# Performance work log

Measured on AMD Instinct MI355X. Metric: run time of the kernel, lower is better.

## Reference

```python
import jax, jax.numpy as jnp
import numpy as np

N_NODES = 50000
N_EDGES = 800000
NODE_IN = 10
EDGE_IN = 7
H = 128
N_LAYERS = 6
OUT_DIM = 3


def setup_inputs() -> dict:
    key = jax.random.key(0)
    ks = jax.random.split(key, 32)
    s = 0.05
    inp = {
        "x": jax.random.normal(ks[0], (N_NODES, NODE_IN), jnp.float32),
        "edge_attr": jax.random.normal(ks[1], (N_EDGES, EDGE_IN), jnp.float32),
        "edge_index": jax.random.randint(ks[2], (2, N_EDGES), 0, N_NODES, jnp.int32),
        "bc_disp": jax.random.uniform(ks[3], (N_NODES, 1), jnp.float32),
        "bc_rot": jax.random.uniform(ks[4], (N_NODES, 1), jnp.float32),
        # node encoder: MLP(10, [H], H)
        "ne_w1": jax.random.normal(ks[5], (NODE_IN, H), jnp.float32) * s,
        "ne_b1": jnp.zeros((H,), jnp.float32),
        "ne_w2": jax.random.normal(ks[6], (H, H), jnp.float32) * s,
        "ne_b2": jnp.zeros((H,), jnp.float32),
        # edge encoder: MLP(7, [H], H)
        "ee_w1": jax.random.normal(ks[7], (EDGE_IN, H), jnp.float32) * s,
        "ee_b1": jnp.zeros((H,), jnp.float32),
        "ee_w2": jax.random.normal(ks[8], (H, H), jnp.float32) * s,
        "ee_b2": jnp.zeros((H,), jnp.float32),
        # 6 GraphNetworkLayers: edge model (3H -> H), node model (2H -> H)
        "mp_ew": jax.random.normal(ks[9], (N_LAYERS, 3 * H, H), jnp.float32) * s,
        "mp_eb": jnp.zeros((N_LAYERS, H), jnp.float32),
        "mp_nw": jax.random.normal(ks[10], (N_LAYERS, 2 * H, H), jnp.float32) * s,
        "mp_nb": jnp.zeros((N_LAYERS, H), jnp.float32),
        "d_w1": jax.random.normal(ks[11], (H, H), jnp.float32) * s,
        "d_b1": jnp.zeros((H,), jnp.float32),
        "d_w2": jax.random.normal(ks[12], (H, 64), jnp.float32) * s,
        "d_b2": jnp.zeros((64,), jnp.float32),
        "d_w3": jax.random.normal(ks[13], (64, OUT_DIM), jnp.float32) * (s * 5.0),
        "d_b3": jnp.full((OUT_DIM,), 0.5, jnp.float32),
    }
    return inp


def reference(x, edge_attr, edge_index, bc_disp, bc_rot,
              ne_w1, ne_b1, ne_w2, ne_b2,
              ee_w1, ee_b1, ee_w2, ee_b2,
              mp_ew, mp_eb, mp_nw, mp_nb,
              d_w1, d_b1, d_w2, d_b2, d_w3, d_b3):
    # encode nodes and edges (Linear -> ReLU -> Linear)
    h = jax.nn.relu(x @ ne_w1 + ne_b1) @ ne_w2 + ne_b2            # [N, H]
    e = jax.nn.relu(edge_attr @ ee_w1 + ee_b1) @ ee_w2 + ee_b2    # [E, H]
    src = edge_index[0]
    dst = edge_index[1]
    # 6 residual message-passing layers: gather -> edge MLP -> scatter-add -> node MLP
    for l in range(N_LAYERS):
        msg_in = jnp.concatenate([h[src], h[dst], e], axis=-1)    # [E, 3H]
        msg = jax.nn.relu(msg_in @ mp_ew[l] + mp_eb[l])           # [E, H]
        agg = jax.ops.segment_sum(msg, dst, num_segments=N_NODES)  # [N, H] (aggr='add')
        upd = jax.nn.relu(jnp.concatenate([h, agg], axis=-1) @ mp_nw[l] + mp_nb[l])
        h = h + upd                                               # residual
    # decode: Linear -> ReLU -> Linear -> ReLU -> Linear
    z = jax.nn.relu(h @ d_w1 + d_b1)
    z = jax.nn.relu(z @ d_w2 + d_b2)
    pred = z @ d_w3 + d_b3                                        # [N, 3]
    # hard boundary conditions
    pred = jnp.concatenate([pred[:, 0:2] * (1.0 - bc_disp),
                            pred[:, 2:3] * (1.0 - bc_rot)], axis=-1)
    return pred
```

## Files before the change

kernel.cpp:

```cpp
#include <hip/hip_runtime.h>
#include <hip/hip_bf16.h>

#define NN 50000
#define NE 800000
#define H 128

typedef __hip_bfloat16 bf16;
typedef __attribute__((ext_vector_type(8))) short short8v;
typedef __attribute__((ext_vector_type(4))) float f32x4;

static __device__ __forceinline__ unsigned short f2bf_bits(float x) {
  union { __hip_bfloat16 b; unsigned short u; } cv;
  cv.b = __float2bfloat16(x);
  return cv.u;
}

__global__ __launch_bounds__(256) void zero_counts_kernel(int* __restrict__ counts) {
  int i = blockIdx.x * 256 + threadIdx.x;
  if (i < NN) counts[i] = 0;
}

__global__ __launch_bounds__(256) void hist_kernel(const int* __restrict__ dstI,
                                                   int* __restrict__ counts) {
  int e = blockIdx.x * 256 + threadIdx.x;
  if (e < NE) atomicAdd(&counts[dstI[e]], 1);
}

__global__ __launch_bounds__(256) void scan_kernel(const int* __restrict__ counts,
                                                   int* __restrict__ cursor) {
  __shared__ int sdata[256];
  __shared__ int sbase;
  const int t = threadIdx.x;
  if (t == 0) sbase = 0;
  __syncthreads();
  for (int c0 = 0; c0 < NN; c0 += 256) {
    int i = c0 + t;
    int v = (i < NN) ? counts[i] : 0;
    sdata[t] = v;
    __syncthreads();
    #pragma unroll
    for (int off = 1; off < 256; off <<= 1) {
      int x = (t >= off) ? sdata[t - off] : 0;
      __syncthreads();
      sdata[t] += x;
      __syncthreads();
    }
    if (i < NN) cursor[i] = sbase + sdata[t] - v;
    __syncthreads();
    if (t == 255) sbase += sdata[255];
    __syncthreads();
  }
}

__global__ __launch_bounds__(256) void scatter_kernel(
    const float* __restrict__ ea, const int* __restrict__ srcI, const int* __restrict__ dstI,
    int* __restrict__ cursor, bf16* __restrict__ eap,
    int* __restrict__ srcp, int* __restrict__ dstp) {
  int e = blockIdx.x * 256 + threadIdx.x;
  if (e >= NE) return;
  int d = dstI[e];
  int pos = atomicAdd(&cursor[d], 1);
  srcp[pos] = srcI[e];
  dstp[pos] = d;
  #pragma unroll
  for (int k = 0; k < 7; ++k) eap[(size_t)pos * 7 + k] = __float2bfloat16(ea[(size_t)e * 7 + k]);
}

__global__ __launch_bounds__(256) void fuse_w3_kernel(
    const float* __restrict__ ee_w2, const float* __restrict__ ee_b2,
    const float* __restrict__ mp_ew, const float* __restrict__ mp_eb,
    float* __restrict__ W3p, float* __restrict__ c3)
{
  const int l = blockIdx.x >> 3;
  const int cc = (blockIdx.x & 7) * 16;
  __shared__ float sA[H * H];
  __shared__ float sB[H * 16];
  const float* W3 = mp_ew + (size_t)l * 384 * H + 256 * H;
  for (int i = threadIdx.x; i < H * H; i += 256) sA[i] = ee_w2[i];
  for (int i = threadIdx.x; i < H * 16; i += 256) {
    int k = i >> 4, j = i & 15;
    sB[i] = W3[k * H + cc + j];
  }
  __syncthreads();
  float* out = W3p + (size_t)l * H * H;
  for (int i = threadIdx.x; i < H * 16; i += 256) {
    int r = i >> 4, j = i & 15;
    float acc = 0.f;
    #pragma unroll 8
    for (int k = 0; k < H; ++k) acc += sA[r * H + k] * sB[k * 16 + j];
    out[r * H + cc + j] = acc;
  }
  if (threadIdx.x < 16) {
    int j = threadIdx.x;
    float acc = mp_eb[l * H + cc + j];
    for (int k = 0; k < H; ++k) acc += ee_b2[k] * sB[k * 16 + j];
    c3[l * H + cc + j] = acc;
  }
}

__global__ __launch_bounds__(256) void repack_w_kernel(
    const float* __restrict__ src0, size_t lstride, bf16* __restrict__ dst0, int K)
{
  const int l = blockIdx.x;
  const float* src = src0 + (size_t)l * lstride;
  bf16* dst = dst0 + (size_t)l * K * 128;
  const int nkk = K / 32;
  const int nslots = 8 * nkk * 64;
  for (int idx = threadIdx.x; idx < nslots; idx += 256) {
    int ng = idx / (nkk * 64);
    int rem = idx % (nkk * 64);
    int kk = rem / 64, ln = rem % 64;
    #pragma unroll
    for (int j = 0; j < 8; ++j) {
      int k = kk * 32 + ((ln >> 4) * 8) + j;
      int col = ng * 16 + (ln & 15);
      dst[(size_t)idx * 8 + j] = __float2bfloat16(src[(size_t)k * 128 + col]);
    }
  }
}

__global__ __launch_bounds__(256) void node_encoder_kernel(
    const float* __restrict__ in,
    const float* __restrict__ w1, const float* __restrict__ b1,
    const float* __restrict__ w2, const float* __restrict__ b2,
    float* __restrict__ out, int nrows)
{
  __shared__ float sw1[10 * H];
  __shared__ float sw2[H * H];
  __shared__ float sb1[H];
  __shared__ float sb2[H];
  __shared__ float sin_[8][10];
  __shared__ float st[8][H];

  for (int i = threadIdx.x; i < 10 * H; i += 256) sw1[i] = w1[i];
  for (int i = threadIdx.x; i < H * H; i += 256) sw2[i] = w2[i];
  if (threadIdx.x < H) { sb1[threadIdx.x] = b1[threadIdx.x]; sb2[threadIdx.x] = b2[threadIdx.x]; }
  __syncthreads();

  const int c = threadIdx.x & 127;
  const int hf = threadIdx.x >> 7;

  for (long long r0 = (long long)blockIdx.x * 8; r0 < nrows; r0 += (long long)gridDim.x * 8) {
    if (threadIdx.x < 80) {
      int j = threadIdx.x / 10, k = threadIdx.x % 10;
      long long r = r0 + j;
      sin_[j][k] = (r < nrows) ? in[r * 10 + k] : 0.f;
    }
    __syncthreads();
    #pragma unroll
    for (int t = 0; t < 4; ++t) {
      int idx = threadIdx.x + t * 256;
      int j = idx >> 7, k = idx & 127;
      float acc = sb1[k];
      #pragma unroll
      for (int i = 0; i < 10; ++i) acc += sin_[j][i] * sw1[i * H + k];
      st[j][k] = fmaxf(acc, 0.f);
    }
    __syncthreads();
    float a0 = sb2[c], a1 = a0, a2 = a0, a3 = a0;
    #pragma unroll 4
    for (int k4 = 0; k4 < H; k4 += 4) {
      float w0 = sw2[(k4 + 0) * H + c];
      float w1v = sw2[(k4 + 1) * H + c];
      float w2v = sw2[(k4 + 2) * H + c];
      float w3v = sw2[(k4 + 3) * H + c];
      float4 s0 = *(const float4*)&st[hf * 4 + 0][k4];
      float4 s1 = *(const float4*)&st[hf * 4 + 1][k4];
      float4 s2 = *(const float4*)&st[hf * 4 + 2][k4];
      float4 s3 = *(const float4*)&st[hf * 4 + 3][k4];
      a0 += s0.x * w0 + s0.y * w1v + s0.z * w2v + s0.w * w3v;
      a1 += s1.x * w0 + s1.y * w1v + s1.z * w2v + s1.w * w3v;
      a2 += s2.x * w0 + s2.y * w1v + s2.z * w2v + s2.w * w3v;
      a3 += s3.x * w0 + s3.y * w1v + s3.z * w2v + s3.w * w3v;
    }
    float accs[4] = {a0, a1, a2, a3};
    #pragma unroll
    for (int j = 0; j < 4; ++j) {
      long long r = r0 + hf * 4 + j;
      if (r < nrows) out[r * H + c] = accs[j];
    }
    __syncthreads();
  }
}

__global__ __launch_bounds__(512) void node_AB_kernel(
    const float* __restrict__ h, const float* __restrict__ W1f, const float* __restrict__ W2f,
    bf16* __restrict__ A, bf16* __restrict__ B, float* __restrict__ agg, int nrows)
{
  __shared__ float sw1[H * H];
  __shared__ float sw2[H * H];
  __shared__ float sh[16][H];
  for (int i = threadIdx.x; i < H * H; i += 512) { sw1[i] = W1f[i]; sw2[i] = W2f[i]; }
  __syncthreads();
  const int c = threadIdx.x & 127;
  const int q = threadIdx.x >> 7;
  for (long long r0 = (long long)blockIdx.x * 16; r0 < nrows; r0 += (long long)gridDim.x * 16) {
    #pragma unroll
    for (int t = 0; t < 4; ++t) {
      int idx = threadIdx.x + t * 512;
      int j = idx >> 7, k = idx & 127;
      long long r = r0 + j;
      sh[j][k] = (r < nrows) ? h[r * H + k] : 0.f;
    }
    __syncthreads();
    float aA[4] = {0, 0, 0, 0}, aB[4] = {0, 0, 0, 0};
    #pragma unroll 2
    for (int k4 = 0; k4 < H; k4 += 4) {
      float w10 = sw1[(k4 + 0) * H + c], w11 = sw1[(k4 + 1) * H + c];
      float w12 = sw1[(k4 + 2) * H + c], w13 = sw1[(k4 + 3) * H + c];
      float w20 = sw2[(k4 + 0) * H + c], w21 = sw2[(k4 + 1) * H + c];
      float w22 = sw2[(k4 + 2) * H + c], w23 = sw2[(k4 + 3) * H + c];
      #pragma unroll
      for (int j = 0; j < 4; ++j) {
        float4 s = *(const float4*)&sh[q * 4 + j][k4];
        aA[j] += s.x * w10 + s.y * w11 + s.z * w12 + s.w * w13;
        aB[j] += s.x * w20 + s.y * w21 + s.z * w22 + s.w * w23;
      }
    }
    #pragma unroll
    for (int j = 0; j < 4; ++j) {
      long long r = r0 + q * 4 + j;
      if (r < nrows) {
        A[r * H + c] = __float2bfloat16(aA[j]);
        B[r * H + c] = __float2bfloat16(aB[j]);
        agg[r * H + c] = 0.f;
      }
    }
    __syncthreads();
  }
}

__global__ __launch_bounds__(512) void edge_mfma_scatter(
    const bf16* __restrict__ eap,
    const int* __restrict__ srcp, const int* __restrict__ dstp,
    const bf16* __restrict__ A, const bf16* __restrict__ B,
    const float* __restrict__ ew1, const float* __restrict__ eb1,
    const bf16* __restrict__ W3b, const float* __restrict__ c3,
    float* __restrict__ agg, int nE)
{
  __shared__ float sew1[7 * H];
  __shared__ float seb1[H];
  __shared__ float sea[64][8];
  __shared__ int   sidx[64];
  __shared__ int   didx[64];
  __shared__ unsigned int shid[64 * 64];
  __shared__ bf16  sAld[64][136];

  for (int i = threadIdx.x; i < 7 * H; i += 512) sew1[i] = ew1[i];
  if (threadIdx.x < H) seb1[threadIdx.x] = eb1[threadIdx.x];

  const int t = threadIdx.x;
  const int lane = t & 63;
  const int wid = t >> 6;
  const int hm = wid >> 2;
  const int colbase = (wid & 3) * 32;

  short8v bfrag[2][4];
  float c3v[2];
  #pragma unroll
  for (int n = 0; n < 2; ++n) {
    c3v[n] = c3[colbase + n * 16 + (lane & 15)];
    int ng = (colbase >> 4) + n;
    #pragma unroll
    for (int kk = 0; kk < 4; ++kk) {
      const bf16* p = W3b + ((size_t)(ng * 4 + kk) * 64 + lane) * 8;
      bfrag[n][kk] = *(const short8v*)p;
    }
  }
  __syncthreads();

  for (long long e0 = (long long)blockIdx.x * 64; e0 < nE; e0 += (long long)gridDim.x * 64) {
    if (t < 448) sea[t / 7][t % 7] = __bfloat162float(eap[e0 * 7 + t]);
    else         sidx[t - 448] = srcp[e0 + (t - 448)];
    if (t < 64)  didx[t] = dstp[e0 + t];
    __syncthreads();

    #pragma unroll
    for (int i = 0; i < 2; ++i) {
      int idx = t + i * 512;
      int el = idx >> 4, seg = idx & 15;
      int s = sidx[el];
      *(short8v*)&sAld[el][seg * 8] = *(const short8v*)&A[(size_t)s * H + seg * 8];
    }

    {
      const int e = t >> 3;
      float r0 = sea[e][0], r1 = sea[e][1], r2 = sea[e][2], r3 = sea[e][3];
      float r4 = sea[e][4], r5 = sea[e][5], r6 = sea[e][6];
      #pragma unroll
      for (int p = 0; p < 8; ++p) {
        int k2 = (t & 7) + 8 * p;
        int k = k2 * 2;
        float a0 = seb1[k], a1 = seb1[k + 1];
        a0 += r0 * sew1[0 * H + k] + r1 * sew1[1 * H + k] + r2 * sew1[2 * H + k]
            + r3 * sew1[3 * H + k] + r4 * sew1[4 * H + k] + r5 * sew1[5 * H + k]
            + r6 * sew1[6 * H + k];
        a1 += r0 * sew1[0 * H + k + 1] + r1 * sew1[1 * H + k + 1] + r2 * sew1[2 * H + k + 1]
            + r3 * sew1[3 * H + k + 1] + r4 * sew1[4 * H + k + 1] + r5 * sew1[5 * H + k + 1]
            + r6 * sew1[6 * H + k + 1];
        a0 = fmaxf(a0, 0.f); a1 = fmaxf(a1, 0.f);
        unsigned int w = (unsigned int)f2bf_bits(a0) | ((unsigned int)f2bf_bits(a1) << 16);
        int off = (e * 256 + k2 * 4) ^ ((e & 7) << 4);
        shid[off >> 2] = w;
      }
    }
    __syncthreads();

    f32x4 acc[2][2];
    const f32x4 z = {0.f, 0.f, 0.f, 0.f};
    acc[0][0] = z; acc[0][1] = z; acc[1][0] = z; acc[1][1] = z;
    #pragma unroll
    for (int m = 0; m < 2; ++m) {
      #pragma unroll
      for (int kk = 0; kk < 4; ++kk) {
        int row = hm * 32 + m * 16 + (lane & 15);
        int off = (row * 256 + kk * 64 + (lane >> 4) * 16) ^ ((row & 7) << 4);
        short8v afrag = *(const short8v*)((const char*)shid + off);
        acc[m][0] = __builtin_amdgcn_mfma_f32_16x16x32_bf16(afrag, bfrag[0][kk], acc[m][0], 0, 0, 0);
        acc[m][1] = __builtin_amdgcn_mfma_f32_16x16x32_bf16(afrag, bfrag[1][kk], acc[m][1], 0, 0, 0);
      }
    }

    const int col0 = colbase + (lane & 15);
    const int col1 = col0 + 16;
    #pragma unroll
    for (int m = 0; m < 2; ++m) {
      float vs0 = 0.f, vs1 = 0.f;
      float b0 = 0.f, b1 = 0.f;
      int dprev = -1;
      #pragma unroll
      for (int r = 0; r < 4; ++r) {
        int el = hm * 32 + m * 16 + (lane >> 4) * 4 + r;
        int d = didx[el];
        if (d != dprev) {
          if (dprev >= 0) {
            atomicAdd(&agg[(size_t)dprev * H + col0], vs0);
            atomicAdd(&agg[(size_t)dprev * H + col1], vs1);
          }
          vs0 = 0.f; vs1 = 0.f;
          b0 = __bfloat162float(B[(size_t)d * H + col0]);
          b1 = __bfloat162float(B[(size_t)d * H + col1]);
          dprev = d;
        }
        float a0v = __bfloat162float(sAld[el][col0]);
        float a1v = __bfloat162float(sAld[el][col1]);
        vs0 += fmaxf(acc[m][0][r] + c3v[0] + a0v + b0, 0.f);
        vs1 += fmaxf(acc[m][1][r] + c3v[1] + a1v + b1, 0.f);
      }
      atomicAdd(&agg[(size_t)dprev * H + col0], vs0);
      atomicAdd(&agg[(size_t)dprev * H + col1], vs1);
    }
    __syncthreads();
  }
}

template<int DO_AB>
__global__ __launch_bounds__(256) void fused_update_kernel(
    float* __restrict__ h, const float* __restrict__ aggin,
    const bf16* __restrict__ Wnb, const float* __restrict__ nb,
    const bf16* __restrict__ W1b, const bf16* __restrict__ W2b,
    bf16* __restrict__ A, bf16* __restrict__ B, float* __restrict__ aggz,
    int nrows)
{
  __shared__ unsigned int sKw[32 * 128];
  unsigned short* shnew = (unsigned short*)sKw;

  const int t = threadIdx.x;
  const int lane = t & 63;
  const int wid = t >> 6;
  const int colbase = wid * 32;

  short8v bU[2][8];
  float nbv[2];
  #pragma unroll
  for (int n = 0; n < 2; ++n) {
    int ng = wid * 2 + n;
    nbv[n] = nb[colbase + n * 16 + (lane & 15)];
    #pragma unroll
    for (int kk = 0; kk < 8; ++kk)
      bU[n][kk] = *(const short8v*)(Wnb + ((size_t)(ng * 8 + kk) * 64 + lane) * 8);
  }

  const int ntiles = (nrows + 31) / 32;
  for (int tile = blockIdx.x; tile < ntiles; tile += gridDim.x) {
    const int r0 = tile * 32;
    #pragma unroll
    for (int i = 0; i < 16; ++i) {
      int w = t + i * 256;
      int row = w >> 7, k2 = w & 127;
      int r = r0 + row;
      float v0 = 0.f, v1 = 0.f;
      if (r < nrows) {
        if (k2 < 64) { float2 p = *(const float2*)&h[(size_t)r * H + 2 * k2]; v0 = p.x; v1 = p.y; }
        else         { float2 p = *(const float2*)&aggin[(size_t)r * H + 2 * k2 - 128]; v0 = p.x; v1 = p.y; }
      }
      unsigned int wrd = (unsigned int)f2bf_bits(v0) | ((unsigned int)f2bf_bits(v1) << 16);
      sKw[((w * 4) ^ ((row & 7) << 4)) >> 2] = wrd;
    }
    __syncthreads();

    f32x4 acc[2][2];
    const f32x4 z = {0.f, 0.f, 0.f, 0.f};
    acc[0][0] = z; acc[0][1] = z; acc[1][0] = z; acc[1][1] = z;
    #pragma unroll
    for (int kk = 0; kk < 8; ++kk) {
      #pragma unroll
      for (int m = 0; m < 2; ++m) {
        int row = m * 16 + (lane & 15);
        int off = (row * 512 + kk * 64 + (lane >> 4) * 16) ^ ((row & 7) << 4);
        short8v afrag = *(const short8v*)((const char*)sKw + off);
        acc[m][0] = __builtin_amdgcn_mfma_f32_16x16x32_bf16(afrag, bU[0][kk], acc[m][0], 0, 0, 0);
        acc[m][1] = __builtin_amdgcn_mfma_f32_16x16x32_bf16(afrag, bU[1][kk], acc[m][1], 0, 0, 0);
      }
    }
    __syncthreads();

    #pragma unroll
    for (int m = 0; m < 2; ++m) {
      #pragma unroll
      for (int r = 0; r < 4; ++r) {
        int row = m * 16 + (lane >> 4) * 4 + r;
        int grow = r0 + row;
        #pragma unroll
        for (int n = 0; n < 2; ++n) {
          int col = colbase + n * 16 + (lane & 15);
          float u = fmaxf(acc[m][n][r] + nbv[n], 0.f);
          float hold = (grow < nrows) ? h[(size_t)grow * H + col] : 0.f;
          float hn = hold + u;
          if (grow < nrows) h[(size_t)grow * H + col] = hn;
          if (DO_AB) {
            int i16 = (row * 128 + col) ^ ((row & 7) << 3);
            shnew[i16] = f2bf_bits(hn);
          }
        }
      }
    }

    if (DO_AB) {
      __syncthreads();
      short8v bA[2][4], bB[2][4];
      #pragma unroll
      for (int n = 0; n < 2; ++n) {
        int ng = wid * 2 + n;
        #pragma unroll
        for (int kk = 0; kk < 4; ++kk) {
          bA[n][kk] = *(const short8v*)(W1b + ((size_t)(ng * 4 + kk) * 64 + lane) * 8);
          bB[n][kk] = *(const short8v*)(W2b + ((size_t)(ng * 4 + kk) * 64 + lane) * 8);
        }
      }
      f32x4 aA[2][2], aB2[2][2];
      aA[0][0] = z; aA[0][1] = z; aA[1][0] = z; aA[1][1] = z;
      aB2[0][0] = z; aB2[0][1] = z; aB2[1][0] = z; aB2[1][1] = z;
      #pragma unroll
      for (int kk = 0; kk < 4; ++kk) {
        #pragma unroll
        for (int m = 0; m < 2; ++m) {
          int row = m * 16 + (lane & 15);
          int off = (row * 256 + kk * 64 + (lane >> 4) * 16) ^ ((row & 7) << 4);
          short8v afrag = *(const short8v*)((const char*)shnew + off);
          aA[m][0] = __builtin_amdgcn_mfma_f32_16x16x32_bf16(afrag, bA[0][kk], aA[m][0], 0, 0, 0);
          aA[m][1] = __builtin_amdgcn_mfma_f32_16x16x32_bf16(afrag, bA[1][kk], aA[m][1], 0, 0, 0);
          aB2[m][0] = __builtin_amdgcn_mfma_f32_16x16x32_bf16(afrag, bB[0][kk], aB2[m][0], 0, 0, 0);
          aB2[m][1] = __builtin_amdgcn_mfma_f32_16x16x32_bf16(afrag, bB[1][kk], aB2[m][1], 0, 0, 0);
        }
      }
      #pragma unroll
      for (int m = 0; m < 2; ++m) {
        #pragma unroll
        for (int r = 0; r < 4; ++r) {
          int row = m * 16 + (lane >> 4) * 4 + r;
          int grow = r0 + row;
          if (grow < nrows) {
            #pragma unroll
            for (int n = 0; n < 2; ++n) {
              int col = colbase + n * 16 + (lane & 15);
              A[(size_t)grow * H + col] = __float2bfloat16(aA[m][n][r]);
              B[(size_t)grow * H + col] = __float2bfloat16(aB2[m][n][r]);
              aggz[(size_t)grow * H + col] = 0.f;
            }
          }
        }
      }
    }
    __syncthreads();
  }
}

__global__ __launch_bounds__(512) void decoder_kernel(
    const float* __restrict__ h,
    const float* __restrict__ w1, const float* __restrict__ b1,
    const float* __restrict__ w2, const float* __restrict__ b2,
    const float* __restrict__ w3, const float* __restrict__ b3,
    const float* __restrict__ bcd, const float* __restrict__ bcr,
    float* __restrict__ out, int nrows)
{
  __shared__ float sw1[H * H];
  __shared__ float sw2[H * 64];
  __shared__ float sw3[64 * 3];
  __shared__ float sb1[H], sb2[64], sb3[3];
  __shared__ float sh[16][H], st1[16][H], st2[16][64];
  for (int i = threadIdx.x; i < H * H; i += 512) sw1[i] = w1[i];
  for (int i = threadIdx.x; i < H * 64; i += 512) sw2[i] = w2[i];
  if (threadIdx.x < 64 * 3) sw3[threadIdx.x] = w3[threadIdx.x];
  if (threadIdx.x < H) sb1[threadIdx.x] = b1[threadIdx.x];
  if (threadIdx.x < 64) sb2[threadIdx.x] = b2[threadIdx.x];
  if (threadIdx.x < 3) sb3[threadIdx.x] = b3[threadIdx.x];
  __syncthreads();
  for (long long r0 = (long long)blockIdx.x * 16; r0 < nrows; r0 += (long long)gridDim.x * 16) {
    #pragma unroll
    for (int t = 0; t < 4; ++t) {
      int idx = threadIdx.x + t * 512;
      int j = idx >> 7, k = idx & 127;
      long long r = r0 + j;
      sh[j][k] = (r < nrows) ? h[r * H + k] : 0.f;
    }
    __syncthreads();
    #pragma unroll
    for (int t = 0; t < 4; ++t) {
      int idx = threadIdx.x + t * 512;
      int j = idx >> 7, k = idx & 127;
      float acc = sb1[k];
      #pragma unroll 8
      for (int i = 0; i < H; ++i) acc += sh[j][i] * sw1[i * H + k];
      st1[j][k] = fmaxf(acc, 0.f);
    }
    __syncthreads();
    #pragma unroll
    for (int t = 0; t < 2; ++t) {
      int idx = threadIdx.x + t * 512;
      int j = idx >> 6, k = idx & 63;
      float acc = sb2[k];
      #pragma unroll 8
      for (int i = 0; i < H; ++i) acc += st1[j][i] * sw2[i * 64 + k];
      st2[j][k] = fmaxf(acc, 0.f);
    }
    __syncthreads();
    if (threadIdx.x < 48) {
      int j = threadIdx.x / 3, o = threadIdx.x % 3;
      float acc = sb3[o];
      #pragma unroll 8
      for (int i = 0; i < 64; ++i) acc += st2[j][i] * sw3[i * 3 + o];
      long long r = r0 + j;
      if (r < nrows) {
        float m = (o < 2) ? (1.f - bcd[r]) : (1.f - bcr[r]);
        out[r * 3 + o] = acc * m;
      }
    }
    __syncthreads();
  }
}

extern "C" void kernel_launch(void* const* d_in, const int* in_sizes, int n_in,
                              void* d_out, int out_size, void* d_ws, size_t ws_size,
                              hipStream_t stream) {
  const float* x     = (const float*)d_in[0];
  const float* ea    = (const float*)d_in[1];
  const int*   eidx  = (const int*)d_in[2];
  const float* bcd   = (const float*)d_in[3];
  const float* bcr   = (const float*)d_in[4];
  const float* ne_w1 = (const float*)d_in[5];
  const float* ne_b1 = (const float*)d_in[6];
  const float* ne_w2 = (const float*)d_in[7];
  const float* ne_b2 = (const float*)d_in[8];
  const float* ee_w1 = (const float*)d_in[9];
  const float* ee_b1 = (const float*)d_in[10];
  const float* ee_w2 = (const float*)d_in[11];
  const float* ee_b2 = (const float*)d_in[12];
  const float* mp_ew = (const float*)d_in[13];
  const float* mp_eb = (const float*)d_in[14];
  const float* mp_nw = (const float*)d_in[15];
  const float* mp_nb = (const float*)d_in[16];
  const float* d_w1  = (const float*)d_in[17];
  const float* d_b1  = (const float*)d_in[18];
  const float* d_w2  = (const float*)d_in[19];
  const float* d_b2  = (const float*)d_in[20];
  const float* d_w3  = (const float*)d_in[21];
  const float* d_b3  = (const float*)d_in[22];

  const int* srcI = eidx;
  const int* dstI = eidx + NE;

  char* wsp = (char*)d_ws;
  float* h    = (float*)wsp; wsp += (size_t)NN * H * 4;
  float* agg  = (float*)wsp; wsp += (size_t)NN * H * 4;
  bf16*  A    = (bf16*)wsp;  wsp += (size_t)NN * H * 2;
  bf16*  B    = (bf16*)wsp;  wsp += (size_t)NN * H * 2;
  bf16*  eap  = (bf16*)wsp;  wsp += (size_t)NE * 7 * 2;
  int*   srcp = (int*)wsp;   wsp += (size_t)NE * 4;
  int*   dstp = (int*)wsp;   wsp += (size_t)NE * 4;
  bf16*  W3b  = (bf16*)wsp;  wsp += (size_t)6 * H * H * 2;
  bf16*  Wnb  = (bf16*)wsp;  wsp += (size_t)6 * 256 * H * 2;
  bf16*  W1b  = (bf16*)wsp;  wsp += (size_t)6 * H * H * 2;
  bf16*  W2b  = (bf16*)wsp;  wsp += (size_t)6 * H * H * 2;
  float* c3   = (float*)wsp; wsp += (size_t)6 * H * 4;
  int*   counts = (int*)A;
  int*   cursor = (int*)A + NN;
  float* W3p    = agg;

  zero_counts_kernel<<<(NN + 255) / 256, 256, 0, stream>>>(counts);
  hist_kernel<<<(NE + 255) / 256, 256, 0, stream>>>(dstI, counts);
  scan_kernel<<<1, 256, 0, stream>>>(counts, cursor);
  scatter_kernel<<<(NE + 255) / 256, 256, 0, stream>>>(ea, srcI, dstI, cursor, eap, srcp, dstp);

  fuse_w3_kernel<<<48, 256, 0, stream>>>(ee_w2, ee_b2, mp_ew, mp_eb, W3p, c3);
  repack_w_kernel<<<6, 256, 0, stream>>>(W3p, (size_t)H * H, W3b, 128);
  repack_w_kernel<<<6, 256, 0, stream>>>(mp_nw, (size_t)256 * H, Wnb, 256);
  repack_w_kernel<<<6, 256, 0, stream>>>(mp_ew, (size_t)384 * H, W1b, 128);
  repack_w_kernel<<<6, 256, 0, stream>>>(mp_ew + 128 * H, (size_t)384 * H, W2b, 128);

  node_encoder_kernel<<<2048, 256, 0, stream>>>(x, ne_w1, ne_b1, ne_w2, ne_b2, h, NN);
  node_AB_kernel<<<1024, 512, 0, stream>>>(h, mp_ew, mp_ew + 128 * H, A, B, agg, NN);

  for (int l = 0; l < 6; ++l) {
    edge_mfma_scatter<<<4096, 512, 0, stream>>>(eap, srcp, dstp, A, B, ee_w1, ee_b1,
                                                W3b + (size_t)l * H * H, c3 + l * H, agg, NE);
    if (l < 5) {
      fused_update_kernel<1><<<512, 256, 0, stream>>>(
          h, agg, Wnb + (size_t)l * 256 * H, mp_nb + l * H,
          W1b + (size_t)(l + 1) * H * H, W2b + (size_t)(l + 1) * H * H,
          A, B, agg, NN);
    } else {
      fused_update_kernel<0><<<512, 256, 0, stream>>>(
          h, agg, Wnb + (size_t)l * 256 * H, mp_nb + l * H,
          nullptr, nullptr, nullptr, nullptr, nullptr, NN);
    }
  }

  decoder_kernel<<<1024, 512, 0, stream>>>(h, d_w1, d_b1, d_w2, d_b2, d_w3, d_b3,
                                           bcd, bcr, (float*)d_out, NN);
}
```

Baseline: 2.786 ms.

## Prefetch next edge tile into registers and enlarge edge/update grids

The edge message kernel now loads the next tile's edge attributes, destination indices and gathered A rows into registers while the current tile is being computed. It then stores them to shared memory at the top of the next iteration, instead of load-sync-gather serially. This hides gather latency behind the MFMA and scatter work. Grid sizes for the edge kernel and the fused node update kernel are also raised, giving more blocks and fewer iterations per block. The prefetch adds register pressure, which may lower occupancy, and with only about two iterations per block the overlap window is small.

```diff
diff --git a/kernel.cpp b/kernel.cpp
--- a/kernel.cpp
+++ b/kernel.cpp
@@ -241,7 +241,6 @@
   __shared__ float sew1[7 * H];
   __shared__ float seb1[H];
   __shared__ float sea[64][8];
-  __shared__ int   sidx[64];
   __shared__ int   didx[64];
   __shared__ unsigned int shid[64 * 64];
   __shared__ bf16  sAld[64][136];
@@ -269,18 +268,39 @@
   }
   __syncthreads();
 
-  for (long long e0 = (long long)blockIdx.x * 64; e0 < nE; e0 += (long long)gridDim.x * 64) {
-    if (t < 448) sea[t / 7][t % 7] = __bfloat162float(eap[e0 * 7 + t]);
-    else         sidx[t - 448] = srcp[e0 + (t - 448)];
-    if (t < 64)  didx[t] = dstp[e0 + t];
-    __syncthreads();
-
-    #pragma unroll
-    for (int i = 0; i < 2; ++i) {
-      int idx = t + i * 512;
-      int el = idx >> 4, seg = idx & 15;
-      int s = sidx[el];
-      *(short8v*)&sAld[el][seg * 8] = *(const short8v*)&A[(size_t)s * H + seg * 8];
+  const long long stride = (long long)gridDim.x * 64;
+  const int elA0 = t >> 4;
+  const int elA1 = 32 + (t >> 4);
+  const int segA = (t & 15) * 8;
+
+  float   pf_ea = 0.f;
+  int     pf_d = 0;
+  short8v pf_A0, pf_A1;
+  long long e0 = (long long)blockIdx.x * 64;
+  if (e0 < nE) {
+    if (t < 448) pf_ea = __bfloat162float(eap[e0 * 7 + t]);
+    if (t < 64)  pf_d = dstp[e0 + t];
+    int s0 = srcp[e0 + elA0];
+    pf_A0 = *(const short8v*)&A[(size_t)s0 * H + segA];
+    int s1 = srcp[e0 + elA1];
+    pf_A1 = *(const short8v*)&A[(size_t)s1 * H + segA];
+  }
+
+  for (; e0 < nE; e0 += stride) {
+    if (t < 448) sea[t / 7][t % 7] = pf_ea;
+    if (t < 64)  didx[t] = pf_d;
+    *(short8v*)&sAld[elA0][segA] = pf_A0;
+    *(short8v*)&sAld[elA1][segA] = pf_A1;
+    __syncthreads();
+
+    long long e1 = e0 + stride;
+    if (e1 < nE) {
+      if (t < 448) pf_ea = __bfloat162float(eap[e1 * 7 + t]);
+      if (t < 64)  pf_d = dstp[e1 + t];
+      int s0 = srcp[e1 + elA0];
+      pf_A0 = *(const short8v*)&A[(size_t)s0 * H + segA];
+      int s1 = srcp[e1 + elA1];
+      pf_A1 = *(const short8v*)&A[(size_t)s1 * H + segA];
     }
 
     {
@@ -612,15 +632,15 @@
   node_AB_kernel<<<1024, 512, 0, stream>>>(h, mp_ew, mp_ew + 128 * H, A, B, agg, NN);
 
   for (int l = 0; l < 6; ++l) {
-    edge_mfma_scatter<<<4096, 512, 0, stream>>>(eap, srcp, dstp, A, B, ee_w1, ee_b1,
+    edge_mfma_scatter<<<6250, 512, 0, stream>>>(eap, srcp, dstp, A, B, ee_w1, ee_b1,
                                                 W3b + (size_t)l * H * H, c3 + l * H, agg, NE);
     if (l < 5) {
-      fused_update_kernel<1><<<512, 256, 0, stream>>>(
+      fused_update_kernel<1><<<1563, 256, 0, stream>>>(
           h, agg, Wnb + (size_t)l * 256 * H, mp_nb + l * H,
           W1b + (size_t)(l + 1) * H * H, W2b + (size_t)(l + 1) * H * H,
           A, B, agg, NN);
     } else {
-      fused_update_kernel<0><<<512, 256, 0, stream>>>(
+      fused_update_kernel<0><<<1563, 256, 0, stream>>>(
           h, agg, Wnb + (size_t)l * 256 * H, mp_nb + l * H,
           nullptr, nullptr, nullptr, nullptr, nullptr, NN);
     }
```

After: 2.797 ms. About the same (+0.4%).
